# Performance work log

Measured on AMD Instinct MI355X. Metric: run time of the kernel, lower is better.

## Reference

```python
import jax, jax.numpy as jnp
import numpy as np

B, S, IN = 32, 512, 19
DE, DD = 256, 128      # encoder / decoder d_model
HE, HD = 8, 4          # heads
LE, LD = 6, 2          # layers
FE, FD = 4 * DE, 4 * DD
EPS = 1e-5


def _ln(x, g, b):
    m = x.mean(-1, keepdims=True)
    v = ((x - m) ** 2).mean(-1, keepdims=True)
    return (x - m) / jnp.sqrt(v + EPS) * g + b


def _mha(x, qkv_w, qkv_b, out_w, out_b, kpad, nh):
    Bq, Sq, D = x.shape
    dh = D // nh
    qkv = x @ qkv_w.T + qkv_b
    q, k, v = jnp.split(qkv, 3, axis=-1)
    hs = lambda t: t.reshape(Bq, Sq, nh, dh).transpose(0, 2, 1, 3)  # -> [B,h,S,dh]
    q, k, v = hs(q), hs(k), hs(v)
    scores = jnp.einsum('bhqd,bhkd->bhqk', q, k) / float(np.sqrt(dh))
    scores = jnp.where(kpad[:, None, None, :], -1e9, scores)  # mask padded keys
    attn = jax.nn.softmax(scores, axis=-1)
    o = jnp.einsum('bhqk,bhkd->bhqd', attn, v).transpose(0, 2, 1, 3).reshape(Bq, Sq, D)
    return o @ out_w.T + out_b


def _block(x, p, kpad, nh):
    qkv_w, qkv_b, ow, ob, f1w, f1b, f2w, f2b, g1, b1, g2, b2 = p
    x = _ln(x + _mha(x, qkv_w, qkv_b, ow, ob, kpad, nh), g1, b1)
    h = jax.nn.relu(x @ f1w.T + f1b) @ f2w.T + f2b
    return _ln(x + h, g2, b2)


def _run(x, ps, kpad, nh, L):
    for i in range(L):
        x = _block(x, tuple(p[i] for p in ps), kpad, nh)
    return x


def _forward(event_tensor, w_in_enc, b_in_enc,
             enc_qkv_w, enc_qkv_b, enc_out_w, enc_out_b,
             enc_f1_w, enc_f1_b, enc_f2_w, enc_f2_b,
             enc_g1, enc_b1, enc_g2, enc_b2,
             mask_token, e2d_w,
             dec_qkv_w, dec_qkv_b, dec_out_w, dec_out_b,
             dec_f1_w, dec_f1_b, dec_f2_w, dec_f2_b,
             dec_g1, dec_b1, dec_g2, dec_b2,
             qh_w, qh_b, dth_w, dth_b,
             attention_mask, pred_mask):
    visible = attention_mask & (~pred_mask)
    counts = visible.sum(axis=1)                                  # [B]
    order = jnp.argsort(~visible, axis=1, stable=True)            # visible positions packed first, in order
    tok = event_tensor @ w_in_enc.T + b_in_enc                    # [B,S,DE]
    vis = jnp.take_along_axis(tok, order[:, :, None], axis=1)
    pos = jnp.arange(S)
    enc_pad = pos[None, :] >= counts[:, None]                      # True = padded slot
    vis = jnp.where(enc_pad[:, :, None], 0.0, vis)
    enc_ps = (enc_qkv_w, enc_qkv_b, enc_out_w, enc_out_b, enc_f1_w, enc_f1_b,
              enc_f2_w, enc_f2_b, enc_g1, enc_b1, enc_g2, enc_b2)
    enc_out = _run(vis, enc_ps, enc_pad, HE, LE)
    dec_vis = enc_out @ e2d_w.T                                    # [B,S,DD]
    idx = jnp.cumsum(visible.astype(jnp.int32), axis=1) - 1        # position -> packed index
    gathered = jnp.take_along_axis(dec_vis, jnp.clip(idx, 0)[:, :, None], axis=1)
    dec_in = jnp.where(visible[:, :, None], gathered, mask_token)  # mask token at masked/pad slots
    dec_ps = (dec_qkv_w, dec_qkv_b, dec_out_w, dec_out_b, dec_f1_w, dec_f1_b,
              dec_f2_w, dec_f2_b, dec_g1, dec_b1, dec_g2, dec_b2)
    dec_out = _run(dec_in, dec_ps, ~attention_mask, HD, LD)
    q = dec_out @ qh_w.T + qh_b
    dt = dec_out @ dth_w.T + dth_b
    return jnp.concatenate([q, dt], axis=-1)                       # [B,S,2]


def setup_inputs():
    key = jax.random.key(0)
    ks = iter(jax.random.split(key, 64))
    nrm = lambda shp, s=0.02: jax.random.normal(next(ks), shp, jnp.float32) * s
    d = {}
    d['event_tensor'] = jax.random.normal(next(ks), (B, S, IN), jnp.float32)
    lengths = jax.random.randint(next(ks), (B,), S // 2, S + 1)
    pos = jnp.arange(S)
    am = pos[None, :] < lengths[:, None]
    pm = (jax.random.uniform(next(ks), (B, S)) < 0.75) & am
    pm = pm.at[:, 0].set(False)  # guarantee >=1 visible token per row
    d['attention_mask'] = am
    d['pred_mask'] = pm
    d['w_in_enc'] = nrm((DE, IN)); d['b_in_enc'] = jnp.zeros((DE,), jnp.float32)
    d['enc_qkv_w'] = nrm((LE, 3 * DE, DE)); d['enc_qkv_b'] = jnp.zeros((LE, 3 * DE), jnp.float32)
    d['enc_out_w'] = nrm((LE, DE, DE));     d['enc_out_b'] = jnp.zeros((LE, DE), jnp.float32)
    d['enc_f1_w'] = nrm((LE, FE, DE));      d['enc_f1_b'] = jnp.zeros((LE, FE), jnp.float32)
    d['enc_f2_w'] = nrm((LE, DE, FE));      d['enc_f2_b'] = jnp.zeros((LE, DE), jnp.float32)
    d['enc_g1'] = jnp.ones((LE, DE), jnp.float32); d['enc_b1'] = jnp.zeros((LE, DE), jnp.float32)
    d['enc_g2'] = jnp.ones((LE, DE), jnp.float32); d['enc_b2'] = jnp.zeros((LE, DE), jnp.float32)
    d['mask_token'] = nrm((DD,))
    d['e2d_w'] = nrm((DD, DE))
    d['dec_qkv_w'] = nrm((LD, 3 * DD, DD)); d['dec_qkv_b'] = jnp.zeros((LD, 3 * DD), jnp.float32)
    d['dec_out_w'] = nrm((LD, DD, DD));     d['dec_out_b'] = jnp.zeros((LD, DD), jnp.float32)
    d['dec_f1_w'] = nrm((LD, FD, DD));      d['dec_f1_b'] = jnp.zeros((LD, FD), jnp.float32)
    d['dec_f2_w'] = nrm((LD, DD, FD));      d['dec_f2_b'] = jnp.zeros((LD, DD), jnp.float32)
    d['dec_g1'] = jnp.ones((LD, DD), jnp.float32); d['dec_b1'] = jnp.zeros((LD, DD), jnp.float32)
    d['dec_g2'] = jnp.ones((LD, DD), jnp.float32); d['dec_b2'] = jnp.zeros((LD, DD), jnp.float32)
    d['qh_w'] = nrm((1, DD));  d['qh_b'] = jnp.zeros((1,), jnp.float32)
    d['dth_w'] = nrm((1, DD)); d['dth_b'] = jnp.zeros((1,), jnp.float32)
    return d


def reference(event_tensor, attention_mask, pred_mask, w_in_enc, b_in_enc,
              enc_qkv_w, enc_qkv_b, enc_out_w, enc_out_b,
              enc_f1_w, enc_f1_b, enc_f2_w, enc_f2_b,
              enc_g1, enc_b1, enc_g2, enc_b2,
              mask_token, e2d_w,
              dec_qkv_w, dec_qkv_b, dec_out_w, dec_out_b,
              dec_f1_w, dec_f1_b, dec_f2_w, dec_f2_b,
              dec_g1, dec_b1, dec_g2, dec_b2,
              qh_w, qh_b, dth_w, dth_b):
    return _forward(event_tensor, w_in_enc, b_in_enc,
                    enc_qkv_w, enc_qkv_b, enc_out_w, enc_out_b,
                    enc_f1_w, enc_f1_b, enc_f2_w, enc_f2_b,
                    enc_g1, enc_b1, enc_g2, enc_b2,
                    mask_token, e2d_w,
                    dec_qkv_w, dec_qkv_b, dec_out_w, dec_out_b,
                    dec_f1_w, dec_f1_b, dec_f2_w, dec_f2_b,
                    dec_g1, dec_b1, dec_g2, dec_b2,
                    qh_w, qh_b, dth_w, dth_b,
                    attention_mask, pred_mask)
```

## Files before the change

### kernel.cpp

```cpp
#include <hip/hip_runtime.h>
#include <hip/hip_bf16.h>

#define B_ 32
#define S_ 512
#define IN_ 19
#define DE_ 256
#define DD_ 128
#define HE_ 8
#define HD_ 4
#define LE_ 6
#define LD_ 2
#define FE_ 1024
#define FD_ 512
#define DH_ 32

typedef __attribute__((ext_vector_type(8))) short short8;
typedef __attribute__((ext_vector_type(4))) float f32x4;

__device__ __forceinline__ short f2bf(float f) {
    union { float f; unsigned u; } x; x.f = f;
    unsigned r = x.u + 0x7fff + ((x.u >> 16) & 1);
    return (short)(r >> 16);
}
__device__ __forceinline__ float bf2f(short s) {
    union { unsigned u; float f; } x; x.u = ((unsigned)(unsigned short)s) << 16;
    return x.f;
}

#define GLL16(g, l) __builtin_amdgcn_global_load_lds( \
    (const __attribute__((address_space(1))) void*)(g), \
    (__attribute__((address_space(3))) void*)(l), 16, 0, 0)

#define QSCALE 0.2550653169f

#define NCONV 9
struct ConvTab {
    const float* src[NCONV];
    short* dst[NCONV];
    int len[NCONV];
};
__global__ __launch_bounds__(256) void conv_kernel(ConvTab tab, int total) {
    int i = blockIdx.x * 256 + threadIdx.x;
    if (i >= total) return;
    int j = i;
    for (int e = 0; e < NCONV; ++e) {
        if (j < tab.len[e]) { tab.dst[e][j] = f2bf(tab.src[e][j]); return; }
        j -= tab.len[e];
    }
}

__global__ __launch_bounds__(S_) void plan_kernel(
    const int* __restrict__ am, const int* __restrict__ pm,
    int* __restrict__ counts, int* __restrict__ lengths, int* __restrict__ order,
    int* __restrict__ visible, int* __restrict__ idx) {
    int b = blockIdx.x, s = threadIdx.x;
    __shared__ int sc[S_];
    int a = (am[b * S_ + s] != 0);
    int v = a && (pm[b * S_ + s] == 0);
    visible[b * S_ + s] = v;
    sc[s] = v | (a << 16);
    __syncthreads();
#pragma unroll
    for (int off = 1; off < S_; off <<= 1) {
        int t = (s >= off) ? sc[s - off] : 0;
        __syncthreads();
        sc[s] += t;
        __syncthreads();
    }
    int incl = sc[s] & 0xffff;
    int tot = sc[S_ - 1];
    int total = tot & 0xffff;
    if (s == 0) { counts[b] = total; lengths[b] = tot >> 16; }
    idx[b * S_ + s] = (incl > 0) ? incl - 1 : 0;
    if (v) order[b * S_ + incl - 1] = s;
    else   order[b * S_ + total + (s - incl)] = s;
}

__global__ __launch_bounds__(DE_) void enc_embed_kernel(
    const float* __restrict__ ev, const float* __restrict__ w, const float* __restrict__ bias,
    const int* __restrict__ counts, const int* __restrict__ order, short* __restrict__ out) {
    int bs = blockIdx.x;
    int b = bs / S_, s = bs % S_;
    int d = threadIdx.x;
    __shared__ float e[IN_];
    bool padded = (s >= counts[b]);
    int src = order[bs];
    if (threadIdx.x < IN_)
        e[threadIdx.x] = padded ? 0.f : ev[(size_t)(b * S_ + src) * IN_ + threadIdx.x];
    __syncthreads();
    float acc = bias[d];
#pragma unroll
    for (int i = 0; i < IN_; ++i) acc += e[i] * w[d * IN_ + i];
    out[(size_t)bs * DE_ + d] = padded ? f2bf(0.f) : f2bf(acc);
}

template <bool RELU, bool QKV>
__global__ __launch_bounds__(256) void gemm_mfma(
    const short* __restrict__ A, const short* __restrict__ Wt, const float* __restrict__ bias,
    short* __restrict__ C, int M, int N, int K,
    short* __restrict__ qb, short* __restrict__ kb, short* __restrict__ vtb, int H, int D,
    const int* __restrict__ live) {
    int bm = blockIdx.y * 64, bn = blockIdx.x * 64;
    if (live && (bm & (S_ - 1)) >= live[bm >> 9]) return;
    __shared__ short As[4][64][32];
    __shared__ short Bs[4][64][32];
    int t = threadIdx.x;
    int wave = t >> 6, lane = t & 63;
    int wm = (wave >> 1) * 32, wn = (wave & 1) * 32;
    int c = lane & 15, quad = lane >> 4;
    f32x4 acc[2][2];
#pragma unroll
    for (int i = 0; i < 2; ++i)
#pragma unroll
        for (int j = 0; j < 2; ++j) acc[i][j] = (f32x4){0.f, 0.f, 0.f, 0.f};

    const short* gA = A + (size_t)(bm + wave * 16 + (lane >> 2)) * K + (lane & 3) * 8;
    const short* gB = Wt + (size_t)(bn + wave * 16 + (lane >> 2)) * K + (lane & 3) * 8;

    for (int k0 = 0; k0 < K; k0 += 128) {
#pragma unroll
        for (int j = 0; j < 4; ++j) {
            GLL16(gA + k0 + j * 32, &As[j][wave * 16][0]);
            GLL16(gB + k0 + j * 32, &Bs[j][wave * 16][0]);
        }
        __syncthreads();
#pragma unroll
        for (int j = 0; j < 4; ++j) {
            short8 a0 = *(const short8*)&As[j][wm + c][quad * 8];
            short8 a1 = *(const short8*)&As[j][wm + 16 + c][quad * 8];
            short8 b0 = *(const short8*)&Bs[j][wn + c][quad * 8];
            short8 b1 = *(const short8*)&Bs[j][wn + 16 + c][quad * 8];
            acc[0][0] = __builtin_amdgcn_mfma_f32_16x16x32_bf16(a0, b0, acc[0][0], 0, 0, 0);
            acc[0][1] = __builtin_amdgcn_mfma_f32_16x16x32_bf16(a0, b1, acc[0][1], 0, 0, 0);
            acc[1][0] = __builtin_amdgcn_mfma_f32_16x16x32_bf16(a1, b0, acc[1][0], 0, 0, 0);
            acc[1][1] = __builtin_amdgcn_mfma_f32_16x16x32_bf16(a1, b1, acc[1][1], 0, 0, 0);
        }
        __syncthreads();
    }
#pragma unroll
    for (int mt = 0; mt < 2; ++mt)
#pragma unroll
        for (int nt = 0; nt < 2; ++nt)
#pragma unroll
            for (int r = 0; r < 4; ++r) {
                int R = bm + wm + mt * 16 + quad * 4 + r;
                int Ncol = bn + wn + nt * 16 + c;
                float v = acc[mt][nt][r] + (bias ? bias[Ncol] : 0.f);
                if (RELU) v = fmaxf(v, 0.f);
                if (!QKV) {
                    C[(size_t)R * N + Ncol] = f2bf(v);
                } else {
                    int s = R & (S_ - 1), b2 = R >> 9;
                    if (Ncol < D) {
                        int h = Ncol >> 5, d = Ncol & 31;
                        qb[(((size_t)b2 * H + h) * S_ + s) * DH_ + d] = f2bf(v * QSCALE);
                    } else if (Ncol < 2 * D) {
                        int n2 = Ncol - D, h = n2 >> 5, d = n2 & 31;
                        kb[(((size_t)b2 * H + h) * S_ + s) * DH_ + d] = f2bf(v);
                    } else {
                        int n2 = Ncol - 2 * D, h = n2 >> 5, d = n2 & 31;
                        vtb[(((size_t)b2 * H + h) * DH_ + d) * S_ + s] = f2bf(v);
                    }
                }
            }
}

__global__ __launch_bounds__(256) void attn_flash(
    const short* __restrict__ qb, const short* __restrict__ kb, const short* __restrict__ vtb,
    const int* __restrict__ limit_arr, const int* __restrict__ qlim,
    short* __restrict__ o, int H, int D) {
    int b = blockIdx.z, h = blockIdx.y;
    if (qlim && (int)(blockIdx.x * 64) >= qlim[b]) return;
    int wave = threadIdx.x >> 6, lane = threadIdx.x & 63;
    int q0 = blockIdx.x * 64 + wave * 16;
    int c = lane & 15, quad = lane >> 4;
    size_t bh = (size_t)b * H + h;
    __shared__ short PtAll[4][16][132];
    short (*Pt)[132] = PtAll[wave];

    f32x4 zero = (f32x4){0.f, 0.f, 0.f, 0.f};
    short8 aq = *(const short8*)&qb[(bh * S_ + q0 + c) * DH_ + quad * 8];
    const short* kbase = kb + bh * S_ * DH_;
    const short* vbase = vtb + bh * DH_ * S_;

    int limit = limit_arr[b];
    int nchunks = (limit + 127) >> 7;

    float lrow[4] = {0.f, 0.f, 0.f, 0.f};
    f32x4 o0 = zero, o1 = zero;

    for (int kc = 0; kc < nchunks; ++kc) {
        f32x4 s[8];
#pragma unroll
        for (int nt = 0; nt < 8; ++nt) {
            short8 bk = *(const short8*)&kbase[(size_t)(kc * 128 + nt * 16 + c) * DH_ + quad * 8];
            s[nt] = __builtin_amdgcn_mfma_f32_16x16x32_bf16(aq, bk, zero, 0, 0, 0);
        }
#pragma unroll
        for (int nt = 0; nt < 8; ++nt) {
            bool ok = (kc * 128 + nt * 16 + c) < limit;
#pragma unroll
            for (int r = 0; r < 4; ++r) {
                float p = ok ? exp2f(s[nt][r]) : 0.f;
                s[nt][r] = p;
                lrow[r] += p;
            }
        }
#pragma unroll
        for (int nt = 0; nt < 8; ++nt)
#pragma unroll
            for (int r = 0; r < 4; ++r)
                Pt[quad * 4 + r][nt * 16 + c] = f2bf(s[nt][r]);
#pragma unroll
        for (int kk = 0; kk < 4; ++kk) {
            short8 ap = *(const short8*)&Pt[c][kk * 32 + quad * 8];
            short8 b0 = *(const short8*)&vbase[(size_t)c * S_ + kc * 128 + kk * 32 + quad * 8];
            short8 b1 = *(const short8*)&vbase[(size_t)(16 + c) * S_ + kc * 128 + kk * 32 + quad * 8];
            o0 = __builtin_amdgcn_mfma_f32_16x16x32_bf16(ap, b0, o0, 0, 0, 0);
            o1 = __builtin_amdgcn_mfma_f32_16x16x32_bf16(ap, b1, o1, 0, 0, 0);
        }
    }
#pragma unroll
    for (int r = 0; r < 4; ++r) {
        float l = lrow[r];
        l += __shfl_xor(l, 1);
        l += __shfl_xor(l, 2);
        l += __shfl_xor(l, 4);
        l += __shfl_xor(l, 8);
        float inv = 1.f / l;
        int row = quad * 4 + r;
        size_t base = (size_t)(b * S_ + q0 + row) * D + h * DH_;
        o[base + c] = f2bf(o0[r] * inv);
        o[base + 16 + c] = f2bf(o1[r] * inv);
    }
}

template <int D>
__global__ __launch_bounds__(64) void add_ln_kernel(
    const short* __restrict__ x, const short* __restrict__ h,
    const float* __restrict__ g, const float* __restrict__ be,
    short* __restrict__ out, const int* __restrict__ live) {
    constexpr int E = D / 64;
    int row = blockIdx.x, t = threadIdx.x;
    if (live && (row & (S_ - 1)) >= live[row >> 9]) return;
    const short* px = x + (size_t)row * D + t * E;
    const short* ph = h + (size_t)row * D + t * E;
    float v[E];
    float s = 0.f;
#pragma unroll
    for (int e = 0; e < E; ++e) {
        v[e] = bf2f(px[e]) + bf2f(ph[e]);
        s += v[e];
    }
#pragma unroll
    for (int off = 32; off; off >>= 1) s += __shfl_xor(s, off, 64);
    float m = s / D;
    float s2 = 0.f;
#pragma unroll
    for (int e = 0; e < E; ++e) {
        float d = v[e] - m;
        s2 += d * d;
    }
#pragma unroll
    for (int off = 32; off; off >>= 1) s2 += __shfl_xor(s2, off, 64);
    float rstd = rsqrtf(s2 / D + 1e-5f);
    short* po = out + (size_t)row * D + t * E;
#pragma unroll
    for (int e = 0; e < E; ++e)
        po[e] = f2bf((v[e] - m) * rstd * g[t * E + e] + be[t * E + e]);
}

__global__ __launch_bounds__(64) void add_ln_head_kernel(
    const short* __restrict__ x, const short* __restrict__ h,
    const float* __restrict__ g, const float* __restrict__ be,
    const float* __restrict__ qw, const float* __restrict__ qb,
    const float* __restrict__ dw, const float* __restrict__ db,
    float* __restrict__ out) {
    int row = blockIdx.x, t = threadIdx.x;
    int d0 = t * 2, d1 = t * 2 + 1;
    float v0 = bf2f(x[(size_t)row * DD_ + d0]) + bf2f(h[(size_t)row * DD_ + d0]);
    float v1 = bf2f(x[(size_t)row * DD_ + d1]) + bf2f(h[(size_t)row * DD_ + d1]);
    float s = v0 + v1;
#pragma unroll
    for (int off = 32; off; off >>= 1) s += __shfl_xor(s, off, 64);
    float m = s / DD_;
    float a0 = v0 - m, a1 = v1 - m;
    float s2 = a0 * a0 + a1 * a1;
#pragma unroll
    for (int off = 32; off; off >>= 1) s2 += __shfl_xor(s2, off, 64);
    float rstd = rsqrtf(s2 / DD_ + 1e-5f);
    float o0 = a0 * rstd * g[d0] + be[d0];
    float o1 = a1 * rstd * g[d1] + be[d1];
    float q = o0 * qw[d0] + o1 * qw[d1];
    float dt = o0 * dw[d0] + o1 * dw[d1];
#pragma unroll
    for (int off = 32; off; off >>= 1) {
        q += __shfl_xor(q, off, 64);
        dt += __shfl_xor(dt, off, 64);
    }
    if (t == 0) {
        out[(size_t)row * 2 + 0] = q + qb[0];
        out[(size_t)row * 2 + 1] = dt + db[0];
    }
}

__global__ __launch_bounds__(DD_) void dec_embed_kernel(
    const short* __restrict__ dec_vis, const float* __restrict__ mask_token,
    const int* __restrict__ visible, const int* __restrict__ idx, short* __restrict__ out) {
    int bs = blockIdx.x, d = threadIdx.x;
    int b = bs / S_;
    short val = visible[bs] ? dec_vis[(size_t)(b * S_ + idx[bs]) * DD_ + d]
                            : f2bf(mask_token[d]);
    out[(size_t)bs * DD_ + d] = val;
}

extern "C" void kernel_launch(void* const* d_in, const int* in_sizes, int n_in,
                              void* d_out, int out_size, void* d_ws, size_t ws_size,
                              hipStream_t stream) {
    const float* ev      = (const float*)d_in[0];
    const int*  am       = (const int*)d_in[1];
    const int*  pm       = (const int*)d_in[2];
    const float* w_in    = (const float*)d_in[3];
    const float* b_in    = (const float*)d_in[4];
    const float* eqkv_w  = (const float*)d_in[5];
    const float* eqkv_b  = (const float*)d_in[6];
    const float* eout_w  = (const float*)d_in[7];
    const float* eout_b  = (const float*)d_in[8];
    const float* ef1_w   = (const float*)d_in[9];
    const float* ef1_b   = (const float*)d_in[10];
    const float* ef2_w   = (const float*)d_in[11];
    const float* ef2_b   = (const float*)d_in[12];
    const float* eg1     = (const float*)d_in[13];
    const float* eb1     = (const float*)d_in[14];
    const float* eg2     = (const float*)d_in[15];
    const float* eb2     = (const float*)d_in[16];
    const float* mask_tok= (const float*)d_in[17];
    const float* e2d_w   = (const float*)d_in[18];
    const float* dqkv_w  = (const float*)d_in[19];
    const float* dqkv_b  = (const float*)d_in[20];
    const float* dout_w  = (const float*)d_in[21];
    const float* dout_b  = (const float*)d_in[22];
    const float* df1_w   = (const float*)d_in[23];
    const float* df1_b   = (const float*)d_in[24];
    const float* df2_w   = (const float*)d_in[25];
    const float* df2_b   = (const float*)d_in[26];
    const float* dg1     = (const float*)d_in[27];
    const float* db1     = (const float*)d_in[28];
    const float* dg2     = (const float*)d_in[29];
    const float* db2     = (const float*)d_in[30];
    const float* qh_w    = (const float*)d_in[31];
    const float* qh_b    = (const float*)d_in[32];
    const float* dth_w   = (const float*)d_in[33];
    const float* dth_b   = (const float*)d_in[34];
    float* out = (float*)d_out;

    const int BS = B_ * S_;
    char* ws = (char*)d_ws;
    int* counts  = (int*)ws;
    int* lengths = counts + 32;
    int* order   = lengths + 32;
    int* visible = order + BS;
    int* idx     = visible + BS;

    short* wb = (short*)(ws + 256 * 1024);
    const int L_eqkv = LE_ * 3 * DE_ * DE_;
    const int L_eout = LE_ * DE_ * DE_;
    const int L_ef1  = LE_ * FE_ * DE_;
    const int L_ef2  = LE_ * DE_ * FE_;
    const int L_e2d  = DD_ * DE_;
    const int L_dqkv = LD_ * 3 * DD_ * DD_;
    const int L_dout = LD_ * DD_ * DD_;
    const int L_df1  = LD_ * FD_ * DD_;
    const int L_df2  = LD_ * DD_ * FD_;
    short* w_eqkv = wb;
    short* w_eout = w_eqkv + L_eqkv;
    short* w_ef1  = w_eout + L_eout;
    short* w_ef2  = w_ef1 + L_ef1;
    short* w_e2d  = w_ef2 + L_ef2;
    short* w_dqkv = w_e2d + L_e2d;
    short* w_dout = w_dqkv + L_dqkv;
    short* w_df1  = w_dout + L_dout;
    short* w_df2  = w_df1 + L_df1;
    const int convTotal = L_eqkv + L_eout + L_ef1 + L_ef2 + L_e2d + L_dqkv + L_dout + L_df1 + L_df2;

    short* bx    = (short*)(ws + 12 * 1024 * 1024);
    short* qbuf  = bx   + (size_t)BS * DE_;
    short* kbuf  = qbuf + (size_t)B_ * HE_ * S_ * DH_;
    short* vtbuf = kbuf + (size_t)B_ * HE_ * S_ * DH_;
    short* battn = vtbuf + (size_t)B_ * HE_ * S_ * DH_;
    short* bt    = battn + (size_t)BS * DE_;
    short* hid   = bt + (size_t)BS * DE_;

    ConvTab tab;
    tab.src[0] = eqkv_w; tab.dst[0] = w_eqkv; tab.len[0] = L_eqkv;
    tab.src[1] = eout_w; tab.dst[1] = w_eout; tab.len[1] = L_eout;
    tab.src[2] = ef1_w;  tab.dst[2] = w_ef1;  tab.len[2] = L_ef1;
    tab.src[3] = ef2_w;  tab.dst[3] = w_ef2;  tab.len[3] = L_ef2;
    tab.src[4] = e2d_w;  tab.dst[4] = w_e2d;  tab.len[4] = L_e2d;
    tab.src[5] = dqkv_w; tab.dst[5] = w_dqkv; tab.len[5] = L_dqkv;
    tab.src[6] = dout_w; tab.dst[6] = w_dout; tab.len[6] = L_dout;
    tab.src[7] = df1_w;  tab.dst[7] = w_df1;  tab.len[7] = L_df1;
    tab.src[8] = df2_w;  tab.dst[8] = w_df2;  tab.len[8] = L_df2;
    conv_kernel<<<(convTotal + 255) / 256, 256, 0, stream>>>(tab, convTotal);

    plan_kernel<<<B_, S_, 0, stream>>>(am, pm, counts, lengths, order, visible, idx);
    enc_embed_kernel<<<BS, DE_, 0, stream>>>(ev, w_in, b_in, counts, order, bx);

    for (int l = 0; l < LE_; ++l) {
        gemm_mfma<false, true><<<dim3(3 * DE_ / 64, BS / 64), 256, 0, stream>>>(
            bx, w_eqkv + (size_t)l * 3 * DE_ * DE_, eqkv_b + (size_t)l * 3 * DE_,
            nullptr, BS, 3 * DE_, DE_, qbuf, kbuf, vtbuf, HE_, DE_, counts);
        attn_flash<<<dim3(S_ / 64, HE_, B_), 256, 0, stream>>>(
            qbuf, kbuf, vtbuf, counts, counts, battn, HE_, DE_);
        gemm_mfma<false, false><<<dim3(DE_ / 64, BS / 64), 256, 0, stream>>>(
            battn, w_eout + (size_t)l * DE_ * DE_, eout_b + (size_t)l * DE_,
            bt, BS, DE_, DE_, nullptr, nullptr, nullptr, 0, 0, counts);
        add_ln_kernel<DE_><<<BS, 64, 0, stream>>>(
            bx, bt, eg1 + (size_t)l * DE_, eb1 + (size_t)l * DE_, bx, counts);
        gemm_mfma<true, false><<<dim3(FE_ / 64, BS / 64), 256, 0, stream>>>(
            bx, w_ef1 + (size_t)l * FE_ * DE_, ef1_b + (size_t)l * FE_,
            hid, BS, FE_, DE_, nullptr, nullptr, nullptr, 0, 0, counts);
        gemm_mfma<false, false><<<dim3(DE_ / 64, BS / 64), 256, 0, stream>>>(
            hid, w_ef2 + (size_t)l * DE_ * FE_, ef2_b + (size_t)l * DE_,
            bt, BS, DE_, FE_, nullptr, nullptr, nullptr, 0, 0, counts);
        add_ln_kernel<DE_><<<BS, 64, 0, stream>>>(
            bx, bt, eg2 + (size_t)l * DE_, eb2 + (size_t)l * DE_, bx, counts);
    }

    gemm_mfma<false, false><<<dim3(DD_ / 64, BS / 64), 256, 0, stream>>>(
        bx, w_e2d, nullptr, bt, BS, DD_, DE_, nullptr, nullptr, nullptr, 0, 0, counts);
    dec_embed_kernel<<<BS, DD_, 0, stream>>>(bt, mask_tok, visible, idx, bx);

    for (int l = 0; l < LD_; ++l) {
        gemm_mfma<false, true><<<dim3(3 * DD_ / 64, BS / 64), 256, 0, stream>>>(
            bx, w_dqkv + (size_t)l * 3 * DD_ * DD_, dqkv_b + (size_t)l * 3 * DD_, nullptr,
            BS, 3 * DD_, DD_, qbuf, kbuf, vtbuf, HD_, DD_, nullptr);
        attn_flash<<<dim3(S_ / 64, HD_, B_), 256, 0, stream>>>(
            qbuf, kbuf, vtbuf, lengths, nullptr, battn, HD_, DD_);
        gemm_mfma<false, false><<<dim3(DD_ / 64, BS / 64), 256, 0, stream>>>(
            battn, w_dout + (size_t)l * DD_ * DD_, dout_b + (size_t)l * DD_,
            bt, BS, DD_, DD_, nullptr, nullptr, nullptr, 0, 0, nullptr);
        add_ln_kernel<DD_><<<BS, 64, 0, stream>>>(
            bx, bt, dg1 + (size_t)l * DD_, db1 + (size_t)l * DD_, bx, nullptr);
        gemm_mfma<true, false><<<dim3(FD_ / 64, BS / 64), 256, 0, stream>>>(
            bx, w_df1 + (size_t)l * FD_ * DD_, df1_b + (size_t)l * FD_,
            hid, BS, FD_, DD_, nullptr, nullptr, nullptr, 0, 0, nullptr);
        gemm_mfma<false, false><<<dim3(DD_ / 64, BS / 64), 256, 0, stream>>>(
            hid, w_df2 + (size_t)l * DD_ * FD_, df2_b + (size_t)l * DD_,
            bt, BS, DD_, FD_, nullptr, nullptr, nullptr, 0, 0, nullptr);
        if (l < LD_ - 1) {
            add_ln_kernel<DD_><<<BS, 64, 0, stream>>>(
                bx, bt, dg2 + (size_t)l * DD_, db2 + (size_t)l * DD_, bx, nullptr);
        } else {
            add_ln_head_kernel<<<BS, 64, 0, stream>>>(
                bx, bt, dg2 + (size_t)l * DD_, db2 + (size_t)l * DD_,
                qh_w, qh_b, dth_w, dth_b, out);
        }
    }
}
```

Measured before the change: 900.8 us.

## Template GEMM tile size, use 32x32 tiles for narrow outputs, fuse conv+plan

Makes the MFMA GEMM templated on tile size and loads one 32-wide K slice per iteration instead of four. The narrow N=256/128 GEMMs now run with 32x32 tiles so they launch more blocks and fill more CUs. The weight-conversion and mask-planning kernels are merged into one launch to save launch overhead. Smaller tiles reduce data reuse, and the K loop now synchronises once per 32 elements instead of once per 128, which adds barrier overhead.

```diff
diff --git a/kernel.cpp b/kernel.cpp
--- a/kernel.cpp
+++ b/kernel.cpp
@@ -39,41 +39,42 @@
     short* dst[NCONV];
     int len[NCONV];
 };
-__global__ __launch_bounds__(256) void conv_kernel(ConvTab tab, int total) {
-    int i = blockIdx.x * 256 + threadIdx.x;
-    if (i >= total) return;
-    int j = i;
-    for (int e = 0; e < NCONV; ++e) {
-        if (j < tab.len[e]) { tab.dst[e][j] = f2bf(tab.src[e][j]); return; }
-        j -= tab.len[e];
-    }
-}
-
-__global__ __launch_bounds__(S_) void plan_kernel(
+__global__ __launch_bounds__(S_) void conv_plan_kernel(
+    ConvTab tab, int total,
     const int* __restrict__ am, const int* __restrict__ pm,
     int* __restrict__ counts, int* __restrict__ lengths, int* __restrict__ order,
     int* __restrict__ visible, int* __restrict__ idx) {
-    int b = blockIdx.x, s = threadIdx.x;
-    __shared__ int sc[S_];
-    int a = (am[b * S_ + s] != 0);
-    int v = a && (pm[b * S_ + s] == 0);
-    visible[b * S_ + s] = v;
-    sc[s] = v | (a << 16);
-    __syncthreads();
-#pragma unroll
-    for (int off = 1; off < S_; off <<= 1) {
-        int t = (s >= off) ? sc[s - off] : 0;
+    if (blockIdx.x < B_) {
+        int b = blockIdx.x, s = threadIdx.x;
+        __shared__ int sc[S_];
+        int a = (am[b * S_ + s] != 0);
+        int v = a && (pm[b * S_ + s] == 0);
+        visible[b * S_ + s] = v;
+        sc[s] = v | (a << 16);
         __syncthreads();
-        sc[s] += t;
-        __syncthreads();
-    }
-    int incl = sc[s] & 0xffff;
-    int tot = sc[S_ - 1];
-    int total = tot & 0xffff;
-    if (s == 0) { counts[b] = total; lengths[b] = tot >> 16; }
-    idx[b * S_ + s] = (incl > 0) ? incl - 1 : 0;
-    if (v) order[b * S_ + incl - 1] = s;
-    else   order[b * S_ + total + (s - incl)] = s;
+#pragma unroll
+        for (int off = 1; off < S_; off <<= 1) {
+            int t = (s >= off) ? sc[s - off] : 0;
+            __syncthreads();
+            sc[s] += t;
+            __syncthreads();
+        }
+        int incl = sc[s] & 0xffff;
+        int tot = sc[S_ - 1];
+        int total2 = tot & 0xffff;
+        if (s == 0) { counts[b] = total2; lengths[b] = tot >> 16; }
+        idx[b * S_ + s] = (incl > 0) ? incl - 1 : 0;
+        if (v) order[b * S_ + incl - 1] = s;
+        else   order[b * S_ + total2 + (s - incl)] = s;
+    } else {
+        int i = (blockIdx.x - B_) * S_ + threadIdx.x;
+        if (i >= total) return;
+        int j = i;
+        for (int e = 0; e < NCONV; ++e) {
+            if (j < tab.len[e]) { tab.dst[e][j] = f2bf(tab.src[e][j]); return; }
+            j -= tab.len[e];
+        }
+    }
 }
 
 __global__ __launch_bounds__(DE_) void enc_embed_kernel(
@@ -94,58 +95,63 @@
     out[(size_t)bs * DE_ + d] = padded ? f2bf(0.f) : f2bf(acc);
 }
 
-template <bool RELU, bool QKV>
+template <int TM, int TN, bool RELU, bool QKV>
 __global__ __launch_bounds__(256) void gemm_mfma(
     const short* __restrict__ A, const short* __restrict__ Wt, const float* __restrict__ bias,
     short* __restrict__ C, int M, int N, int K,
     short* __restrict__ qb, short* __restrict__ kb, short* __restrict__ vtb, int H, int D,
     const int* __restrict__ live) {
-    int bm = blockIdx.y * 64, bn = blockIdx.x * 64;
+    constexpr int HM = TM / 2, HN = TN / 2;
+    constexpr int MI = HM / 16, NI = HN / 16;
+    constexpr int NCHA = TM / 16, NCH = (TM + TN) / 16;
+    int bm = blockIdx.y * TM, bn = blockIdx.x * TN;
     if (live && (bm & (S_ - 1)) >= live[bm >> 9]) return;
-    __shared__ short As[4][64][32];
-    __shared__ short Bs[4][64][32];
+    __shared__ short As[TM][32];
+    __shared__ short Bs[TN][32];
     int t = threadIdx.x;
     int wave = t >> 6, lane = t & 63;
-    int wm = (wave >> 1) * 32, wn = (wave & 1) * 32;
+    int wm = (wave >> 1) * HM, wn = (wave & 1) * HN;
     int c = lane & 15, quad = lane >> 4;
-    f32x4 acc[2][2];
-#pragma unroll
-    for (int i = 0; i < 2; ++i)
-#pragma unroll
-        for (int j = 0; j < 2; ++j) acc[i][j] = (f32x4){0.f, 0.f, 0.f, 0.f};
-
-    const short* gA = A + (size_t)(bm + wave * 16 + (lane >> 2)) * K + (lane & 3) * 8;
-    const short* gB = Wt + (size_t)(bn + wave * 16 + (lane >> 2)) * K + (lane & 3) * 8;
-
-    for (int k0 = 0; k0 < K; k0 += 128) {
-#pragma unroll
-        for (int j = 0; j < 4; ++j) {
-            GLL16(gA + k0 + j * 32, &As[j][wave * 16][0]);
-            GLL16(gB + k0 + j * 32, &Bs[j][wave * 16][0]);
+    f32x4 acc[MI][NI];
+#pragma unroll
+    for (int i = 0; i < MI; ++i)
+#pragma unroll
+        for (int j = 0; j < NI; ++j) acc[i][j] = (f32x4){0.f, 0.f, 0.f, 0.f};
+
+    int srow = lane >> 2, scol = (lane & 3) * 8;
+
+    for (int k0 = 0; k0 < K; k0 += 32) {
+#pragma unroll
+        for (int ch0 = 0; ch0 < NCH; ch0 += 4) {
+            int ch = ch0 + wave;
+            if (ch < NCHA)
+                GLL16(A + (size_t)(bm + ch * 16 + srow) * K + k0 + scol, &As[ch * 16][0]);
+            else
+                GLL16(Wt + (size_t)(bn + (ch - NCHA) * 16 + srow) * K + k0 + scol,
+                      &Bs[(ch - NCHA) * 16][0]);
         }
         __syncthreads();
-#pragma unroll
-        for (int j = 0; j < 4; ++j) {
-            short8 a0 = *(const short8*)&As[j][wm + c][quad * 8];
-            short8 a1 = *(const short8*)&As[j][wm + 16 + c][quad * 8];
-            short8 b0 = *(const short8*)&Bs[j][wn + c][quad * 8];
-            short8 b1 = *(const short8*)&Bs[j][wn + 16 + c][quad * 8];
-            acc[0][0] = __builtin_amdgcn_mfma_f32_16x16x32_bf16(a0, b0, acc[0][0], 0, 0, 0);
-            acc[0][1] = __builtin_amdgcn_mfma_f32_16x16x32_bf16(a0, b1, acc[0][1], 0, 0, 0);
-            acc[1][0] = __builtin_amdgcn_mfma_f32_16x16x32_bf16(a1, b0, acc[1][0], 0, 0, 0);
-            acc[1][1] = __builtin_amdgcn_mfma_f32_16x16x32_bf16(a1, b1, acc[1][1], 0, 0, 0);
-        }
+        short8 av[MI], bv[NI];
+#pragma unroll
+        for (int mi = 0; mi < MI; ++mi) av[mi] = *(const short8*)&As[wm + mi * 16 + c][quad * 8];
+#pragma unroll
+        for (int ni = 0; ni < NI; ++ni) bv[ni] = *(const short8*)&Bs[wn + ni * 16 + c][quad * 8];
+#pragma unroll
+        for (int mi = 0; mi < MI; ++mi)
+#pragma unroll
+            for (int ni = 0; ni < NI; ++ni)
+                acc[mi][ni] = __builtin_amdgcn_mfma_f32_16x16x32_bf16(av[mi], bv[ni], acc[mi][ni], 0, 0, 0);
         __syncthreads();
     }
 #pragma unroll
-    for (int mt = 0; mt < 2; ++mt)
-#pragma unroll
-        for (int nt = 0; nt < 2; ++nt)
+    for (int mi = 0; mi < MI; ++mi)
+#pragma unroll
+        for (int ni = 0; ni < NI; ++ni)
 #pragma unroll
             for (int r = 0; r < 4; ++r) {
-                int R = bm + wm + mt * 16 + quad * 4 + r;
-                int Ncol = bn + wn + nt * 16 + c;
-                float v = acc[mt][nt][r] + (bias ? bias[Ncol] : 0.f);
+                int R = bm + wm + mi * 16 + quad * 4 + r;
+                int Ncol = bn + wn + ni * 16 + c;
+                float v = acc[mi][ni][r] + (bias ? bias[Ncol] : 0.f);
                 if (RELU) v = fmaxf(v, 0.f);
                 if (!QKV) {
                     C[(size_t)R * N + Ncol] = f2bf(v);
@@ -401,51 +407,50 @@
     tab.src[6] = dout_w; tab.dst[6] = w_dout; tab.len[6] = L_dout;
     tab.src[7] = df1_w;  tab.dst[7] = w_df1;  tab.len[7] = L_df1;
     tab.src[8] = df2_w;  tab.dst[8] = w_df2;  tab.len[8] = L_df2;
-    conv_kernel<<<(convTotal + 255) / 256, 256, 0, stream>>>(tab, convTotal);
-
-    plan_kernel<<<B_, S_, 0, stream>>>(am, pm, counts, lengths, order, visible, idx);
+    conv_plan_kernel<<<B_ + (convTotal + S_ - 1) / S_, S_, 0, stream>>>(
+        tab, convTotal, am, pm, counts, lengths, order, visible, idx);
     enc_embed_kernel<<<BS, DE_, 0, stream>>>(ev, w_in, b_in, counts, order, bx);
 
     for (int l = 0; l < LE_; ++l) {
-        gemm_mfma<false, true><<<dim3(3 * DE_ / 64, BS / 64), 256, 0, stream>>>(
+        gemm_mfma<64, 64, false, true><<<dim3(3 * DE_ / 64, BS / 64), 256, 0, stream>>>(
             bx, w_eqkv + (size_t)l * 3 * DE_ * DE_, eqkv_b + (size_t)l * 3 * DE_,
             nullptr, BS, 3 * DE_, DE_, qbuf, kbuf, vtbuf, HE_, DE_, counts);
         attn_flash<<<dim3(S_ / 64, HE_, B_), 256, 0, stream>>>(
             qbuf, kbuf, vtbuf, counts, counts, battn, HE_, DE_);
-        gemm_mfma<false, false><<<dim3(DE_ / 64, BS / 64), 256, 0, stream>>>(
+        gemm_mfma<32, 32, false, false><<<dim3(DE_ / 32, BS / 32), 256, 0, stream>>>(
             battn, w_eout + (size_t)l * DE_ * DE_, eout_b + (size_t)l * DE_,
             bt, BS, DE_, DE_, nullptr, nullptr, nullptr, 0, 0, counts);
         add_ln_kernel<DE_><<<BS, 64, 0, stream>>>(
             bx, bt, eg1 + (size_t)l * DE_, eb1 + (size_t)l * DE_, bx, counts);
-        gemm_mfma<true, false><<<dim3(FE_ / 64, BS / 64), 256, 0, stream>>>(
+        gemm_mfma<64, 64, true, false><<<dim3(FE_ / 64, BS / 64), 256, 0, stream>>>(
             bx, w_ef1 + (size_t)l * FE_ * DE_, ef1_b + (size_t)l * FE_,
             hid, BS, FE_, DE_, nullptr, nullptr, nullptr, 0, 0, counts);
-        gemm_mfma<false, false><<<dim3(DE_ / 64, BS / 64), 256, 0, stream>>>(
+        gemm_mfma<32, 32, false, false><<<dim3(DE_ / 32, BS / 32), 256, 0, stream>>>(
             hid, w_ef2 + (size_t)l * DE_ * FE_, ef2_b + (size_t)l * DE_,
             bt, BS, DE_, FE_, nullptr, nullptr, nullptr, 0, 0, counts);
         add_ln_kernel<DE_><<<BS, 64, 0, stream>>>(
             bx, bt, eg2 + (size_t)l * DE_, eb2 + (size_t)l * DE_, bx, counts);
     }
 
-    gemm_mfma<false, false><<<dim3(DD_ / 64, BS / 64), 256, 0, stream>>>(
+    gemm_mfma<32, 32, false, false><<<dim3(DD_ / 32, BS / 32), 256, 0, stream>>>(
         bx, w_e2d, nullptr, bt, BS, DD_, DE_, nullptr, nullptr, nullptr, 0, 0, counts);
     dec_embed_kernel<<<BS, DD_, 0, stream>>>(bt, mask_tok, visible, idx, bx);
 
     for (int l = 0; l < LD_; ++l) {
-        gemm_mfma<false, true><<<dim3(3 * DD_ / 64, BS / 64), 256, 0, stream>>>(
+        gemm_mfma<64, 64, false, true><<<dim3(3 * DD_ / 64, BS / 64), 256, 0, stream>>>(
             bx, w_dqkv + (size_t)l * 3 * DD_ * DD_, dqkv_b + (size_t)l * 3 * DD_, nullptr,
             BS, 3 * DD_, DD_, qbuf, kbuf, vtbuf, HD_, DD_, nullptr);
         attn_flash<<<dim3(S_ / 64, HD_, B_), 256, 0, stream>>>(
             qbuf, kbuf, vtbuf, lengths, nullptr, battn, HD_, DD_);
-        gemm_mfma<false, false><<<dim3(DD_ / 64, BS / 64), 256, 0, stream>>>(
+        gemm_mfma<32, 32, false, false><<<dim3(DD_ / 32, BS / 32), 256, 0, stream>>>(
             battn, w_dout + (size_t)l * DD_ * DD_, dout_b + (size_t)l * DD_,
             bt, BS, DD_, DD_, nullptr, nullptr, nullptr, 0, 0, nullptr);
         add_ln_kernel<DD_><<<BS, 64, 0, stream>>>(
             bx, bt, dg1 + (size_t)l * DD_, db1 + (size_t)l * DD_, bx, nullptr);
-        gemm_mfma<true, false><<<dim3(FD_ / 64, BS / 64), 256, 0, stream>>>(
+        gemm_mfma<64, 64, true, false><<<dim3(FD_ / 64, BS / 64), 256, 0, stream>>>(
             bx, w_df1 + (size_t)l * FD_ * DD_, df1_b + (size_t)l * FD_,
             hid, BS, FD_, DD_, nullptr, nullptr, nullptr, 0, 0, nullptr);
-        gemm_mfma<false, false><<<dim3(DD_ / 64, BS / 64), 256, 0, stream>>>(
+        gemm_mfma<32, 32, false, false><<<dim3(DD_ / 32, BS / 32), 256, 0, stream>>>(
             hid, w_df2 + (size_t)l * DD_ * FD_, df2_b + (size_t)l * DD_,
             bt, BS, DD_, FD_, nullptr, nullptr, nullptr, 0, 0, nullptr);
         if (l < LD_ - 1) {
```

Measured after the change: 844.3 us. 6.3% less time.
